# Optimization experiments

Measured on AMD Instinct MI355X. Metric: run time of the kernel, lower is better.

The kernel has to match this reference:

```python
import jax, jax.numpy as jnp
import numpy as np

C = 64          # channels
HEADS = 4       # num_heads -> head_dim = 16
HID = int(C * 2.66)  # 170, GDFN hidden channels
B, H, W = 2, 256, 256


def conv1x1(x, w):
    # x: (b,c,h,w), w: (o,c) -> pointwise conv, no bias
    return jnp.einsum('bchw,oc->bohw', x, w)


def dwconv3x3(x, w):
    # depthwise 3x3, SAME padding; w: (C,1,3,3)
    return jax.lax.conv_general_dilated(
        x, w, window_strides=(1, 1), padding='SAME',
        feature_group_count=x.shape[1],
        dimension_numbers=('NCHW', 'OIHW', 'NCHW'))


def layer_norm_c(x, w, b):
    # torch: LayerNorm over channel dim of (b, hw, c), eps=1e-5
    mu = x.mean(axis=1, keepdims=True)
    var = ((x - mu) ** 2).mean(axis=1, keepdims=True)
    xn = (x - mu) / jnp.sqrt(var + 1e-5)
    return xn * w[None, :, None, None] + b[None, :, None, None]


def l2norm(x):
    # F.normalize(dim=-1), eps=1e-12
    n = jnp.sqrt(jnp.sum(x * x, axis=-1, keepdims=True))
    return x / jnp.maximum(n, 1e-12)


def mdta(x, temp, w_qkv, w_qkv_dw, w_po, w_kv, w_kv_dw, w_pof):
    b, c, h, w_ = x.shape
    d = c // HEADS
    qkv = dwconv3x3(conv1x1(x, w_qkv), w_qkv_dw)
    q, k, v = jnp.split(qkv, 3, axis=1)
    rs = lambda t: t.reshape(b, HEADS, d, h * w_)
    q, k, v = l2norm(rs(q)), l2norm(rs(k)), rs(v)
    # channel attention: (b,heads,d,d), softmax over last dim
    attn = jax.nn.softmax(jnp.einsum('bhdn,bhen->bhde', q, k) * temp, axis=-1)
    out = conv1x1(jnp.einsum('bhde,bhen->bhdn', attn, v).reshape(b, c, h, w_), w_po)
    # second gated branch: kv from `out`, reuse attn (qf/kf/attnf are dead code in source)
    kvf = dwconv3x3(conv1x1(out, w_kv), w_kv_dw)
    _kf, vf = jnp.split(kvf, 2, axis=1)
    vf = rs(vf)
    outf = conv1x1(jnp.einsum('bhde,bhen->bhdn', attn, vf).reshape(b, c, h, w_), w_pof)
    return outf


def gdfn(x, w_in, w_dw, w_out):
    x12 = dwconv3x3(conv1x1(x, w_in), w_dw)
    x1, x2 = jnp.split(x12, 2, axis=1)
    return conv1x1(jax.nn.gelu(x1, approximate=False) * x2, w_out)


def setup_inputs() -> dict:
    key = jax.random.key(0)
    ks = jax.random.split(key, 10)
    s = 0.05
    return {
        'x': jax.random.normal(ks[0], (B, C, H, W), jnp.float32),
        'n1_w': jnp.ones((C,), jnp.float32),
        'n1_b': jnp.zeros((C,), jnp.float32),
        'temp': jnp.ones((1, HEADS, 1, 1), jnp.float32),
        'w_qkv': jax.random.normal(ks[1], (3 * C, C), jnp.float32) * s,
        'w_qkv_dw': jax.random.normal(ks[2], (3 * C, 1, 3, 3), jnp.float32) * s,
        'w_po': jax.random.normal(ks[3], (C, C), jnp.float32) * s,
        'w_kv': jax.random.normal(ks[4], (2 * C, C), jnp.float32) * s,
        'w_kv_dw': jax.random.normal(ks[5], (2 * C, 1, 3, 3), jnp.float32) * s,
        'w_pof': jax.random.normal(ks[6], (C, C), jnp.float32) * s,
        'n2_w': jnp.ones((C,), jnp.float32),
        'n2_b': jnp.zeros((C,), jnp.float32),
        'w_in': jax.random.normal(ks[7], (2 * HID, C), jnp.float32) * s,
        'w_dw': jax.random.normal(ks[8], (2 * HID, 1, 3, 3), jnp.float32) * s,
        'w_out': jax.random.normal(ks[9], (C, HID), jnp.float32) * s,
    }


def reference(x, n1_w, n1_b, temp, w_qkv, w_qkv_dw, w_po, w_kv, w_kv_dw, w_pof,
              n2_w, n2_b, w_in, w_dw, w_out):
    x = x + mdta(layer_norm_c(x, n1_w, n1_b), temp,
                 w_qkv, w_qkv_dw, w_po, w_kv, w_kv_dw, w_pof)
    x = x + gdfn(layer_norm_c(x, n2_w, n2_b), w_in, w_dw, w_out)
    return x
```

## Files before the change

kernel.cpp:

```cpp
#include <hip/hip_runtime.h>
#include <hip/hip_bf16.h>
#include <math.h>

#define NPB 65536
#define BATCH 2
#define NTOT (BATCH * NPB)

typedef unsigned short u16;
typedef __attribute__((ext_vector_type(8))) short short8;
typedef __attribute__((ext_vector_type(4))) short short4v;
typedef __attribute__((ext_vector_type(4))) float f32x4;


__device__ __forceinline__ float bf2f(u16 u) {
  union { unsigned u; float f; } v; v.u = ((unsigned)u) << 16; return v.f;
}
__device__ __forceinline__ u16 f2bf(float f) {
  union { float f; unsigned u; } v; v.f = f;
  unsigned r = v.u + 0x7FFFu + ((v.u >> 16) & 1u);
  return (u16)(r >> 16);
}
__device__ __forceinline__ unsigned pk2(float a, float b) {
  return (unsigned)f2bf(a) | ((unsigned)f2bf(b) << 16);
}
__device__ __forceinline__ f32x4 mm(short8 a, short8 b, f32x4 c) {
  return __builtin_amdgcn_mfma_f32_16x16x32_bf16(a, b, c, 0, 0, 0);
}
__device__ __forceinline__ short8 ldfrag(const u16* F, int frag, int l) {
  return *reinterpret_cast<const short8*>(F + ((size_t)frag * 64 + l) * 8);
}
__device__ __forceinline__ void st4(u16* p, f32x4 c) {
  uint2 v; v.x = pk2(c[0], c[1]); v.y = pk2(c[2], c[3]);
  *reinterpret_cast<uint2*>(p) = v;
}
__device__ __forceinline__ float gelu_t(float a) {
  const float z = 0.7978845608f * fmaf(0.044715f * a, a * a, a);
  const float e = __expf(2.f * z);
  const float th = 1.f - 2.f / (e + 1.f);
  return 0.5f * a * (1.f + th);
}

__global__ __launch_bounds__(64) void k_wprep(
    const float* __restrict__ wqkv, const float* __restrict__ win,
    const float* __restrict__ wout, u16* __restrict__ WQf,
    u16* __restrict__ WIf, u16* __restrict__ WOf)
{
  const int f = blockIdx.x;
  const int l = threadIdx.x;
  const int fr = l & 15, fq = l >> 4;
  short8 v;
  u16* dst;
  if (f < 24) {
    const int t = f >> 1, kh = f & 1;
    const int row = t * 16 + fr;
#pragma unroll
    for (int j = 0; j < 8; ++j)
      v[j] = (short)f2bf(wqkv[(size_t)row * 64 + kh * 32 + fq * 8 + j]);
    dst = WQf + ((size_t)f * 64 + l) * 8;
  } else if (f < 68) {
    const int fi = f - 24;
    const int g = fi >> 1, kh = fi & 1;
    const int half = g / 11, t = g % 11;
    const int col = half * 176 + t * 16 + fr;
    const int row = col < 170 ? col : (col < 176 ? -1 : (col < 346 ? col - 6 : -1));
#pragma unroll
    for (int j = 0; j < 8; ++j)
      v[j] = (row < 0) ? (short)0
             : (short)f2bf(win[(size_t)row * 64 + kh * 32 + fq * 8 + j]);
    dst = WIf + ((size_t)fi * 64 + l) * 8;
  } else {
    const int fi = f - 68;
    const int t = fi / 6, kh = fi % 6;
    const int row = t * 16 + fr;
#pragma unroll
    for (int j = 0; j < 8; ++j) {
      const int k = kh * 32 + fq * 8 + j;
      v[j] = (k < 170) ? (short)f2bf(wout[(size_t)row * 170 + k]) : (short)0;
    }
    dst = WOf + ((size_t)fi * 64 + l) * 8;
  }
  *reinterpret_cast<short8*>(dst) = v;
}

__global__ __launch_bounds__(256, 2) void g_lnqkv(
    const float* __restrict__ x, const float* __restrict__ n1w,
    const float* __restrict__ n1b, const u16* __restrict__ WQf,
    u16* __restrict__ qkvp)
{
  const int l = threadIdx.x & 63, fr = l & 15, fq = l >> 4;
  const int wv = blockIdx.x * 4 + (threadIdx.x >> 6);
  const int nw = gridDim.x * 4;
  short8 A[12][2];
#pragma unroll
  for (int t = 0; t < 12; ++t)
#pragma unroll
    for (int kh = 0; kh < 2; ++kh) A[t][kh] = ldfrag(WQf, t * 2 + kh, l);
  float w0[8], g0[8], w1[8], g1[8];
#pragma unroll
  for (int j = 0; j < 8; ++j) {
    w0[j] = n1w[fq * 8 + j];      g0[j] = n1b[fq * 8 + j];
    w1[j] = n1w[32 + fq * 8 + j]; g1[j] = n1b[32 + fq * 8 + j];
  }
  for (int tile = wv; tile < 8192; tile += nw) {
    const size_t n = (size_t)tile * 16 + fr;
    const int b = (int)(n >> 16);
    const int pix = (int)(n & 65535);
    const float* xb = x + ((size_t)b * 64) * NPB + pix;
    float v0[8], v1[8];
    float s = 0.f;
#pragma unroll
    for (int j = 0; j < 8; ++j) { v0[j] = xb[(size_t)(fq * 8 + j) * NPB]; s += v0[j]; }
#pragma unroll
    for (int j = 0; j < 8; ++j) { v1[j] = xb[(size_t)(32 + fq * 8 + j) * NPB]; s += v1[j]; }
    s += __shfl_xor(s, 16); s += __shfl_xor(s, 32);
    const float mu = s * (1.f / 64.f);
    float ss = 0.f;
#pragma unroll
    for (int j = 0; j < 8; ++j) { float d = v0[j] - mu; ss = fmaf(d, d, ss); }
#pragma unroll
    for (int j = 0; j < 8; ++j) { float d = v1[j] - mu; ss = fmaf(d, d, ss); }
    ss += __shfl_xor(ss, 16); ss += __shfl_xor(ss, 32);
    const float rstd = rsqrtf(ss * (1.f / 64.f) + 1e-5f);
    short8 b0, b1;
#pragma unroll
    for (int j = 0; j < 8; ++j) {
      b0[j] = (short)f2bf((v0[j] - mu) * rstd * w0[j] + g0[j]);
      b1[j] = (short)f2bf((v1[j] - mu) * rstd * w1[j] + g1[j]);
    }
    f32x4 c[12];
#pragma unroll
    for (int t = 0; t < 12; ++t) c[t] = f32x4{0.f, 0.f, 0.f, 0.f};
#pragma unroll
    for (int t = 0; t < 12; ++t) c[t] = mm(A[t][0], b0, c[t]);
#pragma unroll
    for (int t = 0; t < 12; ++t) c[t] = mm(A[t][1], b1, c[t]);
#pragma unroll
    for (int t = 0; t < 12; ++t)
      st4(qkvp + ((size_t)t * NTOT + n) * 16 + fq * 4, c[t]);
  }
}

template<int CH, int STRIP>
__global__ __launch_bounds__(256, 2) void k_dwr(
    const u16* __restrict__ in, u16* __restrict__ out,
    const float* __restrict__ wdw, int wofs)
{
  typedef short __attribute__((ext_vector_type(CH))) shortC;
  constexpr int LPP = 16 / CH;
  constexpr int NX  = 256 / LPP;
  constexpr int XC  = 256 / NX;
  const int t = threadIdx.x;
  const int sub = t % LPP, xi = t / LPP;
  const int q = blockIdx.x / XC, xc = blockIdx.x % XC;
  const int strip = blockIdx.y, b = blockIdx.z;
  const int x = xc * NX + xi;
  const int y0 = strip * STRIP;
  const int e0 = sub * CH;
  const int c0 = q * 16 + e0;

  const u16* pin = in + ((size_t)q * NTOT + (size_t)b * NPB) * 16 + e0;

  float w[9][CH];
#pragma unroll
  for (int ch = 0; ch < CH; ++ch) {
    const int row = wofs + c0 + ch;
#pragma unroll
    for (int tap = 0; tap < 9; ++tap)
      w[tap][ch] = wdw[(size_t)row * 9 + tap];
  }

  auto LD = [&](int yy, int xx) -> shortC {
    shortC v;
#pragma unroll
    for (int j = 0; j < CH; ++j) v[j] = 0;
    if ((unsigned)yy < 256u && (unsigned)xx < 256u)
      v = *reinterpret_cast<const shortC*>(pin + (size_t)(yy * 256 + xx) * 16);
    return v;
  };

  shortC r[3][3];
  r[0][0] = LD(y0 - 1, x - 1); r[0][1] = LD(y0 - 1, x); r[0][2] = LD(y0 - 1, x + 1);
  r[1][0] = LD(y0, x - 1);     r[1][1] = LD(y0, x);     r[1][2] = LD(y0, x + 1);

#pragma unroll 2
  for (int yy = 0; yy < STRIP; ++yy) {
    const int y = y0 + yy;
    r[2][0] = LD(y + 1, x - 1); r[2][1] = LD(y + 1, x); r[2][2] = LD(y + 1, x + 1);
    float acc[CH];
#pragma unroll
    for (int ch = 0; ch < CH; ++ch) acc[ch] = 0.f;
#pragma unroll
    for (int ky = 0; ky < 3; ++ky)
#pragma unroll
      for (int kx = 0; kx < 3; ++kx)
#pragma unroll
        for (int ch = 0; ch < CH; ++ch)
          acc[ch] = fmaf(w[ky * 3 + kx][ch], bf2f((u16)r[ky][kx][ch]), acc[ch]);
    u16* po = out + ((size_t)q * NTOT + (size_t)b * NPB +
                     (size_t)(y * 256 + x)) * 16 + e0;
    uint4 o;
    o.x = pk2(acc[0], acc[1]); o.y = pk2(acc[2], acc[3]);
    o.z = pk2(acc[4], acc[5]); o.w = pk2(acc[6], acc[7]);
    *reinterpret_cast<uint4*>(po) = o;
#pragma unroll
    for (int dx = 0; dx < 3; ++dx) { r[0][dx] = r[1][dx]; r[1][dx] = r[2][dx]; }
  }
}

__global__ __launch_bounds__(256, 2) void g_pvdwln(
    const u16* __restrict__ QKV, const u16* __restrict__ Pf,
    const float* __restrict__ wkvd, const u16* __restrict__ M2f,
    const float* __restrict__ x, const float* __restrict__ n2w,
    const float* __restrict__ n2b, u16* __restrict__ X2,
    u16* __restrict__ Y2)
{
  __shared__ __align__(16) u16 sh[336 * 68];
  __shared__ __align__(16) u16 lds_vf[4 * 256 * 16];
  __shared__ __align__(16) u16 swt[9 * 64];
  const int t = threadIdx.x;
  const int tx0 = blockIdx.x * 16, ty0 = blockIdx.y * 16;
  const int b = blockIdx.z;
  const size_t bofs = (size_t)b * NPB;

  for (int i = t; i < 9 * 64; i += 256) {
    const int tap = i >> 6, c = i & 63;
    swt[i] = f2bf(wkvd[((size_t)(64 + c)) * 9 + tap]);
  }

  const int w = t >> 6, l = t & 63, fr = l & 15, fq = l >> 4;
  short8 A[4][2];
#pragma unroll
  for (int tt = 0; tt < 4; ++tt)
#pragma unroll
    for (int kh = 0; kh < 2; ++kh)
      A[tt][kh] = ldfrag(Pf, (b * 4 + tt) * 2 + kh, l);
  const size_t hof = (size_t)(fq & 1) * 8;

  for (int i = w; i < 21; i += 4) {
    const int hidx = i * 16 + fr;
    const int hs = hidx < 323 ? hidx : 323;
    const int py = hs / 18, px = hs % 18;
    const int gy = ty0 + py - 1, gx = tx0 + px - 1;
    const bool ok = ((unsigned)gy < 256u) && ((unsigned)gx < 256u);
    short8 b0, b1;
    if (ok) {
      const size_t pix = bofs + (size_t)(gy * 256 + gx);
      b0 = *reinterpret_cast<const short8*>(
          QKV + ((size_t)(8 + (fq >> 1)) * NTOT + pix) * 16 + hof);
      b1 = *reinterpret_cast<const short8*>(
          QKV + ((size_t)(10 + (fq >> 1)) * NTOT + pix) * 16 + hof);
    } else {
#pragma unroll
      for (int j = 0; j < 8; ++j) { b0[j] = 0; b1[j] = 0; }
    }
    f32x4 c[4];
#pragma unroll
    for (int tt = 0; tt < 4; ++tt) c[tt] = f32x4{0.f, 0.f, 0.f, 0.f};
#pragma unroll
    for (int tt = 0; tt < 4; ++tt) c[tt] = mm(A[tt][0], b0, c[tt]);
#pragma unroll
    for (int tt = 0; tt < 4; ++tt) c[tt] = mm(A[tt][1], b1, c[tt]);
    u16* dp = &sh[hidx * 68];
#pragma unroll
    for (int tt = 0; tt < 4; ++tt) st4(dp + tt * 16 + fq * 4, c[tt]);
  }
  __syncthreads();

  {
    const int sub = t & 3, colx = (t >> 2) & 15, rg = t >> 6;
    const int e0 = sub * 4;
    for (int cb = 0; cb < 4; ++cb) {
      float wf[9][4];
#pragma unroll
      for (int tap = 0; tap < 9; ++tap)
#pragma unroll
        for (int j = 0; j < 4; ++j)
          wf[tap][j] = bf2f(swt[tap * 64 + cb * 16 + e0 + j]);
      short4v rwin[3][3];
      auto LDR = [&](int hr, int slot) {
#pragma unroll
        for (int dx = 0; dx < 3; ++dx)
          rwin[slot][dx] = *reinterpret_cast<const short4v*>(
              &sh[(hr * 18 + colx + dx) * 68 + cb * 16 + e0]);
      };
      const int r0 = rg * 4;
      LDR(r0, 0); LDR(r0 + 1, 1);
#pragma unroll
      for (int k = 0; k < 4; ++k) {
        LDR(r0 + k + 2, (k + 2) % 3);
        const int s0 = k % 3, s1 = (k + 1) % 3, s2 = (k + 2) % 3;
        float acc[4] = {0.f, 0.f, 0.f, 0.f};
#pragma unroll
        for (int dx = 0; dx < 3; ++dx)
#pragma unroll
          for (int j = 0; j < 4; ++j) {
            acc[j] = fmaf(wf[0 + dx][j], bf2f((u16)rwin[s0][dx][j]), acc[j]);
            acc[j] = fmaf(wf[3 + dx][j], bf2f((u16)rwin[s1][dx][j]), acc[j]);
            acc[j] = fmaf(wf[6 + dx][j], bf2f((u16)rwin[s2][dx][j]), acc[j]);
          }
        const int lpix = (r0 + k) * 16 + colx;
        uint2 o; o.x = pk2(acc[0], acc[1]); o.y = pk2(acc[2], acc[3]);
        *reinterpret_cast<uint2*>(&lds_vf[(cb * 256 + lpix) * 16 + e0]) = o;
      }
    }
  }
  __syncthreads();

  {
    short8 Am[4][2];
#pragma unroll
    for (int tt = 0; tt < 4; ++tt)
#pragma unroll
      for (int kh = 0; kh < 2; ++kh)
        Am[tt][kh] = ldfrag(M2f, (b * 4 + tt) * 2 + kh, l);
#pragma unroll
    for (int kk = 0; kk < 4; ++kk) {
      const int row = w * 4 + kk;
      const int lpix = row * 16 + fr;
      const int pix = (ty0 + row) * 256 + tx0 + fr;
      const size_t n = bofs + (size_t)pix;
      const short8 b0 = *reinterpret_cast<const short8*>(
          &lds_vf[((size_t)(fq >> 1) * 256 + lpix) * 16 + hof]);
      const short8 b1 = *reinterpret_cast<const short8*>(
          &lds_vf[((size_t)(2 + (fq >> 1)) * 256 + lpix) * 16 + hof]);
      f32x4 c[4];
#pragma unroll
      for (int tt = 0; tt < 4; ++tt) c[tt] = f32x4{0.f, 0.f, 0.f, 0.f};
#pragma unroll
      for (int tt = 0; tt < 4; ++tt) c[tt] = mm(Am[tt][0], b0, c[tt]);
#pragma unroll
      for (int tt = 0; tt < 4; ++tt) c[tt] = mm(Am[tt][1], b1, c[tt]);
#pragma unroll
      for (int tt = 0; tt < 4; ++tt)
#pragma unroll
        for (int r = 0; r < 4; ++r)
          c[tt][r] += x[((size_t)(b * 64 + tt * 16 + fq * 4 + r)) * NPB + pix];
#pragma unroll
      for (int tt = 0; tt < 4; ++tt)
        st4(X2 + ((size_t)tt * NTOT + n) * 16 + fq * 4, c[tt]);
      float s = 0.f;
#pragma unroll
      for (int tt = 0; tt < 4; ++tt)
#pragma unroll
        for (int r = 0; r < 4; ++r) s += c[tt][r];
      s += __shfl_xor(s, 16); s += __shfl_xor(s, 32);
      const float mu = s * (1.f / 64.f);
      float ss = 0.f;
#pragma unroll
      for (int tt = 0; tt < 4; ++tt)
#pragma unroll
        for (int r = 0; r < 4; ++r) { float d = c[tt][r] - mu; ss = fmaf(d, d, ss); }
      ss += __shfl_xor(ss, 16); ss += __shfl_xor(ss, 32);
      const float rstd = rsqrtf(ss * (1.f / 64.f) + 1e-5f);
#pragma unroll
      for (int tt = 0; tt < 4; ++tt)
#pragma unroll
        for (int r = 0; r < 4; ++r) {
          const int oc = tt * 16 + fq * 4 + r;
          c[tt][r] = (c[tt][r] - mu) * rstd * n2w[oc] + n2b[oc];
        }
#pragma unroll
      for (int tt = 0; tt < 4; ++tt)
        st4(Y2 + ((size_t)tt * NTOT + n) * 16 + fq * 4, c[tt]);
    }
  }
}

__global__ __launch_bounds__(256, 2) void g_windwg(
    const u16* __restrict__ Y2, const u16* __restrict__ WIf,
    const float* __restrict__ wdw, u16* __restrict__ Hg)
{
  __shared__ __align__(16) u16 sy[336 * 72];
  __shared__ __align__(16) u16 sh[336 * 36];
  __shared__ __align__(16) u16 swt[2 * 9 * 176];
  const int t = threadIdx.x;
  const int tx0 = blockIdx.x * 16, ty0 = blockIdx.y * 16;
  const int b = blockIdx.z;
  const size_t bofs = (size_t)b * NPB;

  for (int i = t; i < 2 * 9 * 176; i += 256) {
    const int pl = i / (9 * 176);
    const int r = i % (9 * 176);
    const int tap = r / 176, c = r % 176;
    swt[i] = (c < 170) ? f2bf(wdw[((size_t)(pl * 170 + c)) * 9 + tap]) : (u16)0;
  }
  for (int idx = t; idx < 336; idx += 256) {
    const int py = idx / 18, px = idx % 18;
    const int gy = ty0 + py - 1, gx = tx0 + px - 1;
    const bool ok = (idx < 324) && ((unsigned)gy < 256u) && ((unsigned)gx < 256u);
#pragma unroll
    for (int cb = 0; cb < 4; ++cb) {
      short8 v0, v1;
      if (ok) {
        const u16* src = Y2 + ((size_t)cb * NTOT + bofs + (size_t)(gy * 256 + gx)) * 16;
        v0 = *reinterpret_cast<const short8*>(src);
        v1 = *reinterpret_cast<const short8*>(src + 8);
      } else {
#pragma unroll
        for (int j = 0; j < 8; ++j) { v0[j] = 0; v1[j] = 0; }
      }
      *reinterpret_cast<short8*>(&sy[idx * 72 + cb * 16]) = v0;
      *reinterpret_cast<short8*>(&sy[idx * 72 + cb * 16 + 8]) = v1;
    }
  }
  __syncthreads();

  const int w = t >> 6, l = t & 63, fr = l & 15, fq = l >> 4;
  const int sub = t & 3, colx = (t >> 2) & 15, rg = t >> 6;
  const int e0 = sub * 4;

  for (int q = 0; q < 11; ++q) {
    const short8 a10 = ldfrag(WIf, q * 2, l);
    const short8 a11 = ldfrag(WIf, q * 2 + 1, l);
    const short8 a20 = ldfrag(WIf, (11 + q) * 2, l);
    const short8 a21 = ldfrag(WIf, (11 + q) * 2 + 1, l);
    for (int i = w; i < 21; i += 4) {
      const u16* sp = &sy[(i * 16 + fr) * 72];
      const short8 b0 = *reinterpret_cast<const short8*>(sp + fq * 8);
      const short8 b1 = *reinterpret_cast<const short8*>(sp + 32 + fq * 8);
      f32x4 c1 = {0.f, 0.f, 0.f, 0.f}, c2 = {0.f, 0.f, 0.f, 0.f};
      c1 = mm(a10, b0, c1); c1 = mm(a11, b1, c1);
      c2 = mm(a20, b0, c2); c2 = mm(a21, b1, c2);
      u16* dp = &sh[(i * 16 + fr) * 36];
      st4(dp + fq * 4, c1);
      st4(dp + 16 + fq * 4, c2);
    }
    __syncthreads();

    float wf[2][9][4];
#pragma unroll
    for (int pl = 0; pl < 2; ++pl)
#pragma unroll
      for (int tap = 0; tap < 9; ++tap) {
        const short4v wv = *reinterpret_cast<const short4v*>(
            &swt[(pl * 9 + tap) * 176 + q * 16 + e0]);
#pragma unroll
        for (int j = 0; j < 4; ++j) wf[pl][tap][j] = bf2f((u16)wv[j]);
      }
    short4v rwin[3][3][2];
    auto LDR = [&](int hr, int slot) {
#pragma unroll
      for (int dx = 0; dx < 3; ++dx)
#pragma unroll
        for (int pl = 0; pl < 2; ++pl)
          rwin[slot][dx][pl] = *reinterpret_cast<const short4v*>(
              &sh[(hr * 18 + colx + dx) * 36 + pl * 16 + e0]);
    };
    const int r0 = rg * 4;
    LDR(r0, 0); LDR(r0 + 1, 1);
#pragma unroll
    for (int k = 0; k < 4; ++k) {
      LDR(r0 + k + 2, (k + 2) % 3);
      const int s0 = k % 3, s1 = (k + 1) % 3, s2 = (k + 2) % 3;
      float acc[2][4] = {{0.f, 0.f, 0.f, 0.f}, {0.f, 0.f, 0.f, 0.f}};
#pragma unroll
      for (int pl = 0; pl < 2; ++pl)
#pragma unroll
        for (int dx = 0; dx < 3; ++dx)
#pragma unroll
          for (int j = 0; j < 4; ++j) {
            acc[pl][j] = fmaf(wf[pl][0 + dx][j], bf2f((u16)rwin[s0][dx][pl][j]), acc[pl][j]);
            acc[pl][j] = fmaf(wf[pl][3 + dx][j], bf2f((u16)rwin[s1][dx][pl][j]), acc[pl][j]);
            acc[pl][j] = fmaf(wf[pl][6 + dx][j], bf2f((u16)rwin[s2][dx][pl][j]), acc[pl][j]);
          }
      float v[4];
#pragma unroll
      for (int j = 0; j < 4; ++j) v[j] = gelu_t(acc[0][j]) * acc[1][j];
      const int gy = ty0 + r0 + k, gx = tx0 + colx;
      uint2 o; o.x = pk2(v[0], v[1]); o.y = pk2(v[2], v[3]);
      *reinterpret_cast<uint2*>(
          Hg + ((size_t)q * NTOT + bofs + (size_t)(gy * 256 + gx)) * 16 + e0) = o;
    }
    __syncthreads();
  }
}

__global__ __launch_bounds__(256, 2) void k_gram_p(
    const u16* __restrict__ qkv, float* __restrict__ part)
{
  __shared__ __align__(16) u16 lds[32][520];
  const int chunk = blockIdx.x, h = blockIdx.y, b = blockIdx.z;
  const int t = threadIdx.x;
#pragma unroll
  for (int i = 0; i < 2; ++i) {
    const int p = t + i * 256;
    const size_t pix = (size_t)b * NPB + chunk * 512 + p;
    const u16* srcq = qkv + ((size_t)h * NTOT + pix) * 16;
    const u16* srck = qkv + ((size_t)(4 + h) * NTOT + pix) * 16;
    const short8 q0 = *reinterpret_cast<const short8*>(srcq);
    const short8 q1 = *reinterpret_cast<const short8*>(srcq + 8);
    const short8 k0 = *reinterpret_cast<const short8*>(srck);
    const short8 k1 = *reinterpret_cast<const short8*>(srck + 8);
#pragma unroll
    for (int j = 0; j < 8; ++j) {
      lds[j][p] = (u16)q0[j];  lds[8 + j][p] = (u16)q1[j];
      lds[16 + j][p] = (u16)k0[j]; lds[24 + j][p] = (u16)k1[j];
    }
  }
  __syncthreads();
  const int w = t >> 6, l = t & 63, fr = l & 15, fq = l >> 4;
  if (w >= 3) return;
  float* pp = part + ((size_t)((b * 4 + h) * 128) + chunk) * 288;
  const int rowA = (w == 2) ? 16 + fr : fr;
  const int rowB = (w == 0) ? 16 + fr : rowA;
  f32x4 acc = {0.f, 0.f, 0.f, 0.f};
#pragma unroll
  for (int kt = 0; kt < 16; ++kt) {
    const short8 a  = *reinterpret_cast<const short8*>(&lds[rowA][kt * 32 + fq * 8]);
    const short8 bb = *reinterpret_cast<const short8*>(&lds[rowB][kt * 32 + fq * 8]);
    acc = mm(a, bb, acc);
  }
  if (w == 0) {
#pragma unroll
    for (int r = 0; r < 4; ++r) pp[(fq * 4 + r) * 16 + fr] = acc[r];
  } else if ((fr >> 2) == fq) {
    pp[(w == 1 ? 256 : 272) + fr] = acc[fr & 3];
  }
}

__global__ __launch_bounds__(320) void k_gram_red(
    const float* __restrict__ part, float* __restrict__ G,
    float* __restrict__ Sq, float* __restrict__ Sk)
{
  const int bh = blockIdx.x;
  const int t = threadIdx.x;
  if (t >= 288) return;
  const float* p = part + (size_t)bh * 128 * 288 + t;
  float s = 0.f;
  for (int ch = 0; ch < 128; ++ch) s += p[(size_t)ch * 288];
  const int b = bh >> 2, h = bh & 3;
  if (t < 256) G[bh * 256 + t] = s;
  else if (t < 272) Sq[b * 64 + h * 16 + (t - 256)] = s;
  else Sk[b * 64 + h * 16 + (t - 272)] = s;
}

__global__ __launch_bounds__(256) void k_attn(
    const float* __restrict__ G, const float* __restrict__ Sq,
    const float* __restrict__ Sk, const float* __restrict__ temp,
    const float* __restrict__ wpo, const float* __restrict__ wkv,
    const float* __restrict__ wpof, u16* __restrict__ Pf,
    u16* __restrict__ M2f)
{
  __shared__ float attn[BATCH][4][16][16];
  __shared__ float M1[BATCH][64][64];
  __shared__ float rq[128], rk[128];
  const int t = threadIdx.x;
  if (t < 128) {
    rq[t] = 1.f / fmaxf(sqrtf(Sq[t]), 1e-12f);
    rk[t] = 1.f / fmaxf(sqrtf(Sk[t]), 1e-12f);
  }
  __syncthreads();
  if (t < 128) {
    const int b = t >> 6, h = (t >> 4) & 3, d = t & 15;
    const float tm = temp[h];
    const float* g = G + ((b * 4 + h) * 16 + d) * 16;
    const float rqd = rq[b * 64 + h * 16 + d];
    float L[16], mx = -1e30f;
#pragma unroll
    for (int e = 0; e < 16; ++e) {
      L[e] = g[e] * rqd * rk[b * 64 + h * 16 + e] * tm;
      mx = fmaxf(mx, L[e]);
    }
    float s = 0.f;
#pragma unroll
    for (int e = 0; e < 16; ++e) { L[e] = expf(L[e] - mx); s += L[e]; }
    const float inv = 1.f / s;
#pragma unroll
    for (int e = 0; e < 16; ++e) attn[b][h][d][e] = L[e] * inv;
  }
  __syncthreads();
  for (int s0 = 0; s0 < 32; ++s0) {
    const int idx = t * 32 + s0;
    const int b = idx >> 12, o = (idx >> 6) & 63, c = idx & 63;
    const int h = c >> 4, e = c & 15;
    float a = 0.f;
#pragma unroll
    for (int d = 0; d < 16; ++d) a = fmaf(wpo[o * 64 + h * 16 + d], attn[b][h][d][e], a);
    M1[b][o][c] = a;
  }
  __syncthreads();
  for (int it = 0; it < 4; ++it) {
    const int idx = it * 256 + t;
    const int l = idx & 63;
    const int fi = idx >> 6;
    const int b = fi >> 3, tt = (fi >> 1) & 3, kh = fi & 1;
    const int fr = l & 15, fq = l >> 4;
    const int o = tt * 16 + fr;
    short8 pv, mv;
#pragma unroll
    for (int j = 0; j < 8; ++j) {
      const int c = kh * 32 + fq * 8 + j;
      const int h = c >> 4, e = c & 15;
      float a2 = 0.f;
#pragma unroll
      for (int d = 0; d < 16; ++d)
        a2 = fmaf(wpof[o * 64 + h * 16 + d], attn[b][h][d][e], a2);
      mv[j] = (short)f2bf(a2);
      float a = 0.f;
      for (int jj = 0; jj < 64; ++jj)
        a = fmaf(wkv[(64 + o) * 64 + jj], M1[b][jj][c], a);
      pv[j] = (short)f2bf(a);
    }
    *reinterpret_cast<short8*>(Pf + ((size_t)fi * 64 + l) * 8) = pv;
    *reinterpret_cast<short8*>(M2f + ((size_t)fi * 64 + l) * 8) = mv;
  }
}

__global__ __launch_bounds__(256, 2) void g_out(
    const u16* __restrict__ hg, const u16* __restrict__ WOf,
    const u16* __restrict__ X2, float* __restrict__ out)
{
  const int l = threadIdx.x & 63, fr = l & 15, fq = l >> 4;
  const int wv = blockIdx.x * 4 + (threadIdx.x >> 6);
  const int nw = gridDim.x * 4;
  short8 A[4][6];
#pragma unroll
  for (int t = 0; t < 4; ++t)
#pragma unroll
    for (int kh = 0; kh < 6; ++kh)
      A[t][kh] = ldfrag(WOf, t * 6 + kh, l);
  const size_t hof = (size_t)(fq & 1) * 8;
  for (int tile = wv; tile < 8192; tile += nw) {
    const size_t n = (size_t)tile * 16 + fr;
    short8 bb[6];
#pragma unroll
    for (int kh = 0; kh < 6; ++kh) {
      int hb = kh * 2 + (fq >> 1);
      if (hb > 10) hb = 10;
      bb[kh] = *reinterpret_cast<const short8*>(
          hg + ((size_t)hb * NTOT + n) * 16 + hof);
    }
    f32x4 c[4];
#pragma unroll
    for (int t = 0; t < 4; ++t) c[t] = f32x4{0.f, 0.f, 0.f, 0.f};
#pragma unroll
    for (int kh = 0; kh < 6; ++kh)
#pragma unroll
      for (int t = 0; t < 4; ++t) c[t] = mm(A[t][kh], bb[kh], c[t]);
    const int b = (int)(n >> 16);
    const int pix = (int)(n & 65535);
#pragma unroll
    for (int t = 0; t < 4; ++t) {
      const uint2 xv = *reinterpret_cast<const uint2*>(
          X2 + ((size_t)t * NTOT + n) * 16 + fq * 4);
      const u16 h0 = (u16)(xv.x & 0xffff), h1 = (u16)(xv.x >> 16);
      const u16 h2 = (u16)(xv.y & 0xffff), h3 = (u16)(xv.y >> 16);
      const int ocb = b * 64 + t * 16 + fq * 4;
      out[((size_t)(ocb + 0)) * NPB + pix] = c[t][0] + bf2f(h0);
      out[((size_t)(ocb + 1)) * NPB + pix] = c[t][1] + bf2f(h1);
      out[((size_t)(ocb + 2)) * NPB + pix] = c[t][2] + bf2f(h2);
      out[((size_t)(ocb + 3)) * NPB + pix] = c[t][3] + bf2f(h3);
    }
  }
}

extern "C" void kernel_launch(void* const* d_in, const int* in_sizes, int n_in,
                              void* d_out, int out_size, void* d_ws, size_t ws_size,
                              hipStream_t stream)
{
  const float* x     = (const float*)d_in[0];
  const float* n1w   = (const float*)d_in[1];
  const float* n1b   = (const float*)d_in[2];
  const float* temp  = (const float*)d_in[3];
  const float* wqkv  = (const float*)d_in[4];
  const float* wqkvd = (const float*)d_in[5];
  const float* wpo   = (const float*)d_in[6];
  const float* wkv   = (const float*)d_in[7];
  const float* wkvd  = (const float*)d_in[8];
  const float* wpof  = (const float*)d_in[9];
  const float* n2w   = (const float*)d_in[10];
  const float* n2b   = (const float*)d_in[11];
  const float* win   = (const float*)d_in[12];
  const float* wdw   = (const float*)d_in[13];
  const float* wout  = (const float*)d_in[14];
  float* out = (float*)d_out;

  char* ws = (char*)d_ws;
  const size_t offA  = 0;
  const size_t offB  = 16777216;
  const size_t offC  = offB + 50331648;
  const size_t offHg = offC + 50331648;
  const size_t offX2 = offHg + 46137344 + 256;
  const size_t offSm = offX2 + 16777216;

  u16* Y2   = (u16*)(ws + offA);
  u16* QKVp = (u16*)(ws + offB);
  u16* QKV  = (u16*)(ws + offC);
  u16* Hg   = (u16*)(ws + offHg);
  u16* X2   = (u16*)(ws + offX2);
  float* part = (float*)(ws + offSm);
  float* G    = (float*)(ws + offSm + 1179648);
  float* Sq   = (float*)(ws + offSm + 1179648 + 8192);
  float* Sk   = (float*)(ws + offSm + 1179648 + 8704);
  u16* Pf     = (u16*)(ws + offSm + 1179648 + 9216);
  u16* M2f    = (u16*)(ws + offSm + 1179648 + 25600);
  u16* WQf    = (u16*)(ws + offSm + 1179648 + 41984);
  u16* WIf    = (u16*)(ws + offSm + 1179648 + 66560);
  u16* WOf    = (u16*)(ws + offSm + 1179648 + 111616);

  k_wprep<<<dim3(92), 64, 0, stream>>>(wqkv, win, wout, WQf, WIf, WOf);
  g_lnqkv<<<dim3(512), 256, 0, stream>>>(x, n1w, n1b, WQf, QKVp);
  k_dwr<8, 16><<<dim3(24, 16, BATCH), 256, 0, stream>>>(QKVp, QKV, wqkvd, 0);
  k_gram_p<<<dim3(128, 4, BATCH), 256, 0, stream>>>(QKV, part);
  k_gram_red<<<dim3(BATCH * 4), 320, 0, stream>>>(part, G, Sq, Sk);
  k_attn<<<dim3(1), 256, 0, stream>>>(G, Sq, Sk, temp, wpo, wkv, wpof, Pf, M2f);
  g_pvdwln<<<dim3(16, 16, BATCH), 256, 0, stream>>>(
      QKV, Pf, wkvd, M2f, x, n2w, n2b, X2, Y2);
  g_windwg<<<dim3(16, 16, BATCH), 256, 0, stream>>>(Y2, WIf, wdw, Hg);
  g_out<<<dim3(512), 256, 0, stream>>>(Hg, WOf, X2, out);
}
```

Before: 216.1 us.

## Compute GDFN depthwise 3x3 conv with MFMA using diagonal weight fragments

Replaces the scalar FMA depthwise 3x3 conv in the GDFN kernel with MFMA ops. Weights are pre-packed once into sparse diagonal bf16 fragments, so each MFMA covers two taps across 16 channels, and per-block LDS weight staging is removed. This trades VALU FMAs and bf16 conversions for MFMA work that is mostly multiplies by zero. It also changes the LDS access pattern for the tile reads.

```diff
diff --git a/kernel.cpp b/kernel.cpp
--- a/kernel.cpp
+++ b/kernel.cpp
@@ -42,8 +42,9 @@
 
 __global__ __launch_bounds__(64) void k_wprep(
     const float* __restrict__ wqkv, const float* __restrict__ win,
-    const float* __restrict__ wout, u16* __restrict__ WQf,
-    u16* __restrict__ WIf, u16* __restrict__ WOf)
+    const float* __restrict__ wout, const float* __restrict__ wdw,
+    u16* __restrict__ WQf, u16* __restrict__ WIf, u16* __restrict__ WOf,
+    u16* __restrict__ WDf)
 {
   const int f = blockIdx.x;
   const int l = threadIdx.x;
@@ -68,7 +69,7 @@
       v[j] = (row < 0) ? (short)0
              : (short)f2bf(win[(size_t)row * 64 + kh * 32 + fq * 8 + j]);
     dst = WIf + ((size_t)fi * 64 + l) * 8;
-  } else {
+  } else if (f < 92) {
     const int fi = f - 68;
     const int t = fi / 6, kh = fi % 6;
     const int row = t * 16 + fr;
@@ -78,6 +79,20 @@
       v[j] = (k < 170) ? (short)f2bf(wout[(size_t)row * 170 + k]) : (short)0;
     }
     dst = WOf + ((size_t)fi * 64 + l) * 8;
+  } else {
+    const int fd = f - 92;
+    const int pl = fd / 55, rest = fd % 55;
+    const int p = rest / 11, q = rest % 11;
+    const int tap = 2 * p + (fq >> 1);
+    const int c = q * 16 + fr;
+    const int ts = tap < 9 ? tap : 0;
+    const int cs = c < 170 ? c : 0;
+    const float wv = wdw[((size_t)(pl * 170 + cs)) * 9 + ts];
+    const bool act = (tap < 9) && (c < 170) && ((fq & 1) == (fr >> 3));
+#pragma unroll
+    for (int j = 0; j < 8; ++j)
+      v[j] = (act && j == (fr & 7)) ? (short)f2bf(wv) : (short)0;
+    dst = WDf + ((size_t)fd * 64 + l) * 8;
   }
   *reinterpret_cast<short8*>(dst) = v;
 }
@@ -368,22 +383,15 @@
 
 __global__ __launch_bounds__(256, 2) void g_windwg(
     const u16* __restrict__ Y2, const u16* __restrict__ WIf,
-    const float* __restrict__ wdw, u16* __restrict__ Hg)
+    const u16* __restrict__ WDf, u16* __restrict__ Hg)
 {
   __shared__ __align__(16) u16 sy[336 * 72];
   __shared__ __align__(16) u16 sh[336 * 36];
-  __shared__ __align__(16) u16 swt[2 * 9 * 176];
   const int t = threadIdx.x;
   const int tx0 = blockIdx.x * 16, ty0 = blockIdx.y * 16;
   const int b = blockIdx.z;
   const size_t bofs = (size_t)b * NPB;
 
-  for (int i = t; i < 2 * 9 * 176; i += 256) {
-    const int pl = i / (9 * 176);
-    const int r = i % (9 * 176);
-    const int tap = r / 176, c = r % 176;
-    swt[i] = (c < 170) ? f2bf(wdw[((size_t)(pl * 170 + c)) * 9 + tap]) : (u16)0;
-  }
   for (int idx = t; idx < 336; idx += 256) {
     const int py = idx / 18, px = idx % 18;
     const int gy = ty0 + py - 1, gx = tx0 + px - 1;
@@ -406,8 +414,6 @@
   __syncthreads();
 
   const int w = t >> 6, l = t & 63, fr = l & 15, fq = l >> 4;
-  const int sub = t & 3, colx = (t >> 2) & 15, rg = t >> 6;
-  const int e0 = sub * 4;
 
   for (int q = 0; q < 11; ++q) {
     const short8 a10 = ldfrag(WIf, q * 2, l);
@@ -427,49 +433,41 @@
     }
     __syncthreads();
 
-    float wf[2][9][4];
-#pragma unroll
-    for (int pl = 0; pl < 2; ++pl)
-#pragma unroll
-      for (int tap = 0; tap < 9; ++tap) {
-        const short4v wv = *reinterpret_cast<const short4v*>(
-            &swt[(pl * 9 + tap) * 176 + q * 16 + e0]);
-#pragma unroll
-        for (int j = 0; j < 4; ++j) wf[pl][tap][j] = bf2f((u16)wv[j]);
+    short8 AD0[5], AD1[5];
+#pragma unroll
+    for (int p = 0; p < 5; ++p) {
+      AD0[p] = ldfrag(WDf, p * 11 + q, l);
+      AD1[p] = ldfrag(WDf, 55 + p * 11 + q, l);
+    }
+#pragma unroll
+    for (int gi = 0; gi < 4; ++gi) {
+      const int g = w + gi * 4;
+      f32x4 ac1 = {0.f, 0.f, 0.f, 0.f}, ac2 = {0.f, 0.f, 0.f, 0.f};
+#pragma unroll
+      for (int p = 0; p < 5; ++p) {
+        int tap = 2 * p + (fq >> 1);
+        if (tap > 8) tap = 8;
+        const int pos = (g + tap / 3) * 18 + fr + tap % 3;
+        const u16* bp = &sh[pos * 36 + (fq & 1) * 8];
+        const short4v l0 = *reinterpret_cast<const short4v*>(bp);
+        const short4v h0 = *reinterpret_cast<const short4v*>(bp + 4);
+        const short4v l1 = *reinterpret_cast<const short4v*>(bp + 16);
+        const short4v h1 = *reinterpret_cast<const short4v*>(bp + 20);
+        short8 b0v, b1v;
+        b0v[0] = l0[0]; b0v[1] = l0[1]; b0v[2] = l0[2]; b0v[3] = l0[3];
+        b0v[4] = h0[0]; b0v[5] = h0[1]; b0v[6] = h0[2]; b0v[7] = h0[3];
+        b1v[0] = l1[0]; b1v[1] = l1[1]; b1v[2] = l1[2]; b1v[3] = l1[3];
+        b1v[4] = h1[0]; b1v[5] = h1[1]; b1v[6] = h1[2]; b1v[7] = h1[3];
+        ac1 = mm(AD0[p], b0v, ac1);
+        ac2 = mm(AD1[p], b1v, ac2);
       }
-    short4v rwin[3][3][2];
-    auto LDR = [&](int hr, int slot) {
-#pragma unroll
-      for (int dx = 0; dx < 3; ++dx)
-#pragma unroll
-        for (int pl = 0; pl < 2; ++pl)
-          rwin[slot][dx][pl] = *reinterpret_cast<const short4v*>(
-              &sh[(hr * 18 + colx + dx) * 36 + pl * 16 + e0]);
-    };
-    const int r0 = rg * 4;
-    LDR(r0, 0); LDR(r0 + 1, 1);
-#pragma unroll
-    for (int k = 0; k < 4; ++k) {
-      LDR(r0 + k + 2, (k + 2) % 3);
-      const int s0 = k % 3, s1 = (k + 1) % 3, s2 = (k + 2) % 3;
-      float acc[2][4] = {{0.f, 0.f, 0.f, 0.f}, {0.f, 0.f, 0.f, 0.f}};
-#pragma unroll
-      for (int pl = 0; pl < 2; ++pl)
-#pragma unroll
-        for (int dx = 0; dx < 3; ++dx)
-#pragma unroll
-          for (int j = 0; j < 4; ++j) {
-            acc[pl][j] = fmaf(wf[pl][0 + dx][j], bf2f((u16)rwin[s0][dx][pl][j]), acc[pl][j]);
-            acc[pl][j] = fmaf(wf[pl][3 + dx][j], bf2f((u16)rwin[s1][dx][pl][j]), acc[pl][j]);
-            acc[pl][j] = fmaf(wf[pl][6 + dx][j], bf2f((u16)rwin[s2][dx][pl][j]), acc[pl][j]);
-          }
       float v[4];
 #pragma unroll
-      for (int j = 0; j < 4; ++j) v[j] = gelu_t(acc[0][j]) * acc[1][j];
-      const int gy = ty0 + r0 + k, gx = tx0 + colx;
+      for (int j = 0; j < 4; ++j) v[j] = gelu_t(ac1[j]) * ac2[j];
+      const int gy = ty0 + g, gx = tx0 + fr;
       uint2 o; o.x = pk2(v[0], v[1]); o.y = pk2(v[2], v[3]);
       *reinterpret_cast<uint2*>(
-          Hg + ((size_t)q * NTOT + bofs + (size_t)(gy * 256 + gx)) * 16 + e0) = o;
+          Hg + ((size_t)q * NTOT + bofs + (size_t)(gy * 256 + gx)) * 16 + fq * 4) = o;
     }
     __syncthreads();
   }
@@ -697,8 +695,9 @@
   u16* WQf    = (u16*)(ws + offSm + 1179648 + 41984);
   u16* WIf    = (u16*)(ws + offSm + 1179648 + 66560);
   u16* WOf    = (u16*)(ws + offSm + 1179648 + 111616);
-
-  k_wprep<<<dim3(92), 64, 0, stream>>>(wqkv, win, wout, WQf, WIf, WOf);
+  u16* WDf    = (u16*)(ws + offSm + 1179648 + 136192);
+
+  k_wprep<<<dim3(202), 64, 0, stream>>>(wqkv, win, wout, wdw, WQf, WIf, WOf, WDf);
   g_lnqkv<<<dim3(512), 256, 0, stream>>>(x, n1w, n1b, WQf, QKVp);
   k_dwr<8, 16><<<dim3(24, 16, BATCH), 256, 0, stream>>>(QKVp, QKV, wqkvd, 0);
   k_gram_p<<<dim3(128, 4, BATCH), 256, 0, stream>>>(QKV, part);
@@ -706,6 +705,6 @@
   k_attn<<<dim3(1), 256, 0, stream>>>(G, Sq, Sk, temp, wpo, wkv, wpof, Pf, M2f);
   g_pvdwln<<<dim3(16, 16, BATCH), 256, 0, stream>>>(
       QKV, Pf, wkvd, M2f, x, n2w, n2b, X2, Y2);
-  g_windwg<<<dim3(16, 16, BATCH), 256, 0, stream>>>(Y2, WIf, wdw, Hg);
+  g_windwg<<<dim3(16, 16, BATCH), 256, 0, stream>>>(Y2, WIf, WDf, Hg);
   g_out<<<dim3(512), 256, 0, stream>>>(Hg, WOf, X2, out);
 }
```

After: 206.7 us. -4.3%, faster.
